# Performance work log

Measured on AMD Instinct MI355X. Metric: run time of the kernel, lower is better.

## Reference

```python
import jax, jax.numpy as jnp
import numpy as np

EMBED_DIM = 768
NUM_HEADS = 12
HEAD_DIM = EMBED_DIM // NUM_HEADS


def setup_inputs() -> dict:
    key = jax.random.key(0)
    ks = jax.random.split(key, 9)
    B, N, D = 8, 1024, EMBED_DIM
    s = 1.0 / np.sqrt(D)
    x = jax.random.normal(ks[0], (B, N, D), dtype=jnp.float32)
    Wq = jax.random.normal(ks[1], (D, D), dtype=jnp.float32) * s
    bq = jnp.zeros((D,), dtype=jnp.float32)
    Wk = jax.random.normal(ks[2], (D, D), dtype=jnp.float32) * s
    bk = jnp.zeros((D,), dtype=jnp.float32)
    Wv = jax.random.normal(ks[3], (D, D), dtype=jnp.float32) * s
    bv = jnp.zeros((D,), dtype=jnp.float32)
    Wo = jax.random.normal(ks[4], (D, D), dtype=jnp.float32) * s
    bo = jnp.zeros((D,), dtype=jnp.float32)
    return {"x": x, "Wq": Wq, "bq": bq, "Wk": Wk, "bk": bk,
            "Wv": Wv, "bv": bv, "Wo": Wo, "bo": bo}


def reference(x, Wq, bq, Wk, bk, Wv, bv, Wo, bo):
    B, N, D = x.shape
    H, Hd = NUM_HEADS, HEAD_DIM
    # torch Linear: y = x @ W.T + b
    q = (x @ Wq.T + bq).reshape(B, N, H, Hd).transpose(0, 2, 1, 3)  # [B,H,N,Hd]
    k = (x @ Wk.T + bk).reshape(B, N, H, Hd).transpose(0, 2, 1, 3)
    v = (x @ Wv.T + bv).reshape(B, N, H, Hd).transpose(0, 2, 1, 3)
    # NOTE: original scales by embed_dim**-0.5 (not head_dim)
    scale = jnp.asarray(D, x.dtype) ** -0.5
    scores = jnp.einsum('bhnd,bhmd->bhnm', q, k) * scale  # [B,H,N,N]
    attn = jax.nn.softmax(scores, axis=-1)
    out = jnp.einsum('bhnm,bhmd->bhnd', attn, v)  # dropout: identity in eval
    out = out.transpose(0, 2, 1, 3).reshape(B, N, D)
    return out @ Wo.T + bo
```

## Files before the change

### kernel.cpp

```cpp
#include <hip/hip_runtime.h>
#include <math.h>


typedef __bf16 bf16x8 __attribute__((ext_vector_type(8)));
typedef float  f32x4  __attribute__((ext_vector_type(4)));
typedef unsigned u32x2 __attribute__((ext_vector_type(2)));
typedef unsigned u32x4 __attribute__((ext_vector_type(4)));
typedef unsigned short ushort_t;

__device__ __forceinline__ unsigned short f2bf(float f) {
    unsigned u = __float_as_uint(f);
    u += 0x7fffu + ((u >> 16) & 1u);
    return (unsigned short)(u >> 16);
}
__device__ __forceinline__ unsigned pk16(unsigned short lo, unsigned short hi) {
    return (unsigned)lo | ((unsigned)hi << 16);
}

#define GLL16(g, l)                                                                        \
    __builtin_amdgcn_global_load_lds((const __attribute__((address_space(1))) void*)(g),   \
                                     (__attribute__((address_space(3))) void*)(l), 16, 0, 0)

__global__ __launch_bounds__(256)
void cast_all(const float* __restrict__ x,
              const float* __restrict__ w0, const float* __restrict__ w1,
              const float* __restrict__ w2, const float* __restrict__ w3,
              ushort_t* __restrict__ xb, ushort_t* __restrict__ wb0,
              ushort_t* __restrict__ wb1, ushort_t* __restrict__ wb2,
              ushort_t* __restrict__ wb3)
{
    const int y = blockIdx.y;
    const float* s; ushort_t* d; int n;
    switch (y) {
        case 0:  s = x;  d = xb;  n = 8192 * 768; break;
        case 1:  s = w0; d = wb0; n = 768 * 768;  break;
        case 2:  s = w1; d = wb1; n = 768 * 768;  break;
        case 3:  s = w2; d = wb2; n = 768 * 768;  break;
        default: s = w3; d = wb3; n = 768 * 768;  break;
    }
    const int i = (blockIdx.x * 256 + threadIdx.x) * 8;
    if (i >= n) return;
    const float4 f0 = *(const float4*)(s + i);
    const float4 f1 = *(const float4*)(s + i + 4);
    ushort4 p0, p1;
    p0.x = f2bf(f0.x); p0.y = f2bf(f0.y); p0.z = f2bf(f0.z); p0.w = f2bf(f0.w);
    p1.x = f2bf(f1.x); p1.y = f2bf(f1.y); p1.z = f2bf(f1.z); p1.w = f2bf(f1.w);
    *(ushort4*)(d + i)     = p0;
    *(ushort4*)(d + i + 4) = p1;
}

__global__ __launch_bounds__(256, 3)
void gemm_qkv(const ushort_t* __restrict__ xb,
              const ushort_t* __restrict__ wqb, const ushort_t* __restrict__ wkb,
              const ushort_t* __restrict__ wvb,
              const float* __restrict__ bq, const float* __restrict__ bk,
              const float* __restrict__ bv,
              ushort_t* __restrict__ Qh, ushort_t* __restrict__ Kl,
              ushort_t* __restrict__ Vl)
{
    __shared__ ushort_t smem[14336];
    ushort_t* As  = smem;
    ushort_t* Ws0 = smem + 2048;
    ushort_t* Ws1 = smem + 6144;
    ushort_t* Ws2 = smem + 10240;

    const int tid = threadIdx.x, L = tid & 63, wv = tid >> 6;
    const int c = L & 15, g = L >> 4;
    const int n0 = blockIdx.x * 128, m0 = blockIdx.y * 64;

    const int qs = ((tid & 3) ^ ((tid >> 3) & 3)) * 8;
    const ushort_t* ap = xb  + (size_t)(m0 + (tid >> 2)) * 768 + qs;
    const ushort_t* wq = wqb + (size_t)(n0 + (tid >> 2)) * 768 + qs;
    const ushort_t* wk = wkb + (size_t)(n0 + (tid >> 2)) * 768 + qs;
    const ushort_t* wvp = wvb + (size_t)(n0 + (tid >> 2)) * 768 + qs;
    const size_t st64 = (size_t)64 * 768;
    const int sg = (g ^ ((c >> 1) & 3)) * 8;

    f32x4 acc[3][4][2];
#pragma unroll
    for (int z = 0; z < 3; ++z)
#pragma unroll
        for (int i = 0; i < 4; ++i)
#pragma unroll
            for (int j = 0; j < 2; ++j) acc[z][i][j] = (f32x4){0.f, 0.f, 0.f, 0.f};

    for (int k0 = 0; k0 < 768; k0 += 32) {
        __syncthreads();
        GLL16(ap + k0,          &As[(size_t)tid * 8]);
        GLL16(wq + k0,          &Ws0[(size_t)tid * 8]);
        GLL16(wq + st64 + k0,   &Ws0[(size_t)(tid + 256) * 8]);
        GLL16(wk + k0,          &Ws1[(size_t)tid * 8]);
        GLL16(wk + st64 + k0,   &Ws1[(size_t)(tid + 256) * 8]);
        GLL16(wvp + k0,         &Ws2[(size_t)tid * 8]);
        GLL16(wvp + st64 + k0,  &Ws2[(size_t)(tid + 256) * 8]);
        __syncthreads();
        bf16x8 af[4];
#pragma unroll
        for (int i = 0; i < 4; ++i)
            af[i] = *(const bf16x8*)&As[(i * 16 + c) * 32 + sg];
        bf16x8 bf[3][2];
        const ushort_t* wsz[3] = {Ws0, Ws1, Ws2};
#pragma unroll
        for (int z = 0; z < 3; ++z)
#pragma unroll
            for (int j = 0; j < 2; ++j)
                bf[z][j] = *(const bf16x8*)&wsz[z][(wv * 32 + j * 16 + c) * 32 + sg];
#pragma unroll
        for (int z = 0; z < 3; ++z)
#pragma unroll
            for (int i = 0; i < 4; ++i)
#pragma unroll
                for (int j = 0; j < 2; ++j)
                    acc[z][i][j] = __builtin_amdgcn_mfma_f32_16x16x32_bf16(
                        af[i], bf[z][j], acc[z][i][j], 0, 0, 0);
    }

    const int b  = m0 >> 10, nb = m0 & 1023;
    const int hcol = n0 + wv * 32;
    const int h = hcol >> 6, uh = (hcol >> 5) & 1;
    const int bh = b * 12 + h;
    ushort_t* scr = smem + wv * 2304;

    float bias2[3][2];
#pragma unroll
    for (int j = 0; j < 2; ++j) {
        bias2[0][j] = bq[hcol + j * 16 + c];
        bias2[1][j] = bk[hcol + j * 16 + c];
        bias2[2][j] = bv[hcol + j * 16 + c];
    }

    __syncthreads();

#pragma unroll
    for (int i = 0; i < 4; ++i)
#pragma unroll
        for (int j = 0; j < 2; ++j)
#pragma unroll
            for (int r = 0; r < 4; ++r)
                scr[(i * 16 + g * 4 + r) * 36 + j * 16 + c] =
                    f2bf(acc[0][i][j][r] + bias2[0][j]);
#pragma unroll
    for (int e = 0; e < 4; ++e) {
        const int slot = e * 64 + L;
        const int row = slot >> 2, ch = slot & 3;
        const u32x4 v = *(const u32x4*)&scr[row * 36 + ch * 8];
        *(u32x4*)&Qh[((size_t)bh * 1024 + nb + row) * 64 + uh * 32 + ch * 8] = v;
    }

#pragma unroll
    for (int i = 0; i < 4; ++i)
#pragma unroll
        for (int j = 0; j < 2; ++j)
#pragma unroll
            for (int r = 0; r < 4; ++r)
                scr[(i * 16 + g * 4 + r) * 36 + j * 16 + c] =
                    f2bf(acc[1][i][j][r] + bias2[1][j]);
#pragma unroll
    for (int tau = 0; tau < 4; ++tau) {
        const u32x4 v = *(const u32x4*)&scr[(tau * 16 + c) * 36 + g * 8];
        *(u32x4*)&Kl[(((size_t)bh * 64 + (nb >> 4) + tau) * 2 + uh) * 512
                     + (size_t)L * 8] = v;
    }

#pragma unroll
    for (int i = 0; i < 4; ++i)
#pragma unroll
        for (int j = 0; j < 2; ++j)
#pragma unroll
            for (int r = 0; r < 4; ++r)
                scr[(j * 16 + c) * 68 + i * 16 + g * 4 + r] =
                    f2bf(acc[2][i][j][r] + bias2[2][j]);
    const int T = nb >> 6;
#pragma unroll
    for (int t = 0; t < 4; ++t) {
        const int htl = t >> 1, u = t & 1;
        const u32x4 v = *(const u32x4*)&scr[(htl * 16 + c) * 68 + u * 32 + g * 8];
        *(u32x4*)&Vl[((((size_t)bh * 4 + uh * 2 + htl) * 16 + T) * 2 + u) * 512
                     + (size_t)L * 8] = v;
    }
}

__global__ __launch_bounds__(256, 3)
void gemm_outp(const ushort_t* __restrict__ attnb, const ushort_t* __restrict__ wob,
               const float* __restrict__ bo, float* __restrict__ out)
{
    __shared__ ushort_t smem[6144];
    ushort_t* As = smem;
    ushort_t* Ws = smem + 2048;
    const int tid = threadIdx.x, L = tid & 63, wv = tid >> 6;
    const int c = L & 15, g = L >> 4;
    const int n0 = blockIdx.x * 128, m0 = blockIdx.y * 64;
    const int qs = ((tid & 3) ^ ((tid >> 3) & 3)) * 8;
    const ushort_t* ap = attnb + (size_t)(m0 + (tid >> 2)) * 768 + qs;
    const ushort_t* wp = wob   + (size_t)(n0 + (tid >> 2)) * 768 + qs;
    const size_t st64 = (size_t)64 * 768;
    const int sg = (g ^ ((c >> 1) & 3)) * 8;

    f32x4 acc[4][2];
#pragma unroll
    for (int i = 0; i < 4; ++i)
#pragma unroll
        for (int j = 0; j < 2; ++j) acc[i][j] = (f32x4){0.f, 0.f, 0.f, 0.f};

    for (int k0 = 0; k0 < 768; k0 += 32) {
        __syncthreads();
        GLL16(ap + k0,        &As[(size_t)tid * 8]);
        GLL16(wp + k0,        &Ws[(size_t)tid * 8]);
        GLL16(wp + st64 + k0, &Ws[(size_t)(tid + 256) * 8]);
        __syncthreads();
        bf16x8 af[4], bf[2];
#pragma unroll
        for (int i = 0; i < 4; ++i)
            af[i] = *(const bf16x8*)&As[(i * 16 + c) * 32 + sg];
#pragma unroll
        for (int j = 0; j < 2; ++j)
            bf[j] = *(const bf16x8*)&Ws[(wv * 32 + j * 16 + c) * 32 + sg];
#pragma unroll
        for (int i = 0; i < 4; ++i)
#pragma unroll
            for (int j = 0; j < 2; ++j)
                acc[i][j] = __builtin_amdgcn_mfma_f32_16x16x32_bf16(
                    af[i], bf[j], acc[i][j], 0, 0, 0);
    }

#pragma unroll
    for (int i = 0; i < 4; ++i) {
        const int row = m0 + i * 16 + g * 4;
#pragma unroll
        for (int j = 0; j < 2; ++j) {
            const int col = n0 + wv * 32 + j * 16 + c;
            const float bsvo = bo[col];
#pragma unroll
            for (int r = 0; r < 4; ++r)
                out[(size_t)(row + r) * 768 + col] = acc[i][j][r] + bsvo;
        }
    }
}

__global__ __launch_bounds__(64, 3)
void flash_bf16(const ushort_t* __restrict__ Q, const ushort_t* __restrict__ Kl,
                const ushort_t* __restrict__ Vl, ushort_t* __restrict__ attnb)
{
    __shared__ ushort_t Ps[2][2][16 * 68];
    const int L = threadIdx.x;
    const int c = L & 15, g = L >> 4;
    const int bh = blockIdx.x, q0 = blockIdx.y * 32;
    const float SC2 = 0.05205954985329743f;

    const ushort_t* Qp = Q + ((size_t)bh * 1024 + q0 + c) * 64 + g * 8;
    bf16x8 qf[2][2];
    qf[0][0] = *(const bf16x8*)Qp;
    qf[0][1] = *(const bf16x8*)(Qp + 32);
    qf[1][0] = *(const bf16x8*)(Qp + 16 * 64);
    qf[1][1] = *(const bf16x8*)(Qp + 16 * 64 + 32);

    const ushort_t* Kb = Kl + (size_t)bh * 65536 + (size_t)L * 8;
    const ushort_t* Vb = Vl + (size_t)bh * 65536 + (size_t)L * 8;

    f32x4 o[2][4];
#pragma unroll
    for (int w = 0; w < 2; ++w)
#pragma unroll
        for (int ht = 0; ht < 4; ++ht) o[w][ht] = (f32x4){0.f, 0.f, 0.f, 0.f};
    float ls[2] = {0.f, 0.f};

    bf16x8 kf0[4], kf1[4];
#pragma unroll
    for (int ct = 0; ct < 4; ++ct) {
        kf0[ct] = *(const bf16x8*)(Kb + (size_t)(ct * 2 + 0) * 512);
        kf1[ct] = *(const bf16x8*)(Kb + (size_t)(ct * 2 + 1) * 512);
    }

    for (int T0 = 0; T0 < 16; T0 += 2) {
#pragma unroll
        for (int p = 0; p < 2; ++p) {
            const int T = T0 + p;
            bf16x8 vf0[4], vf1[4];
#pragma unroll
            for (int ht = 0; ht < 4; ++ht) {
                const ushort_t* vp = Vb + (size_t)((ht * 16 + T) * 2) * 512;
                vf0[ht] = *(const bf16x8*)vp;
                vf1[ht] = *(const bf16x8*)(vp + 512);
            }
            f32x4 s[2][4];
#pragma unroll
            for (int w = 0; w < 2; ++w)
#pragma unroll
                for (int ct = 0; ct < 4; ++ct) {
                    f32x4 zz = (f32x4){0.f, 0.f, 0.f, 0.f};
                    zz = __builtin_amdgcn_mfma_f32_16x16x32_bf16(kf0[ct], qf[w][0], zz, 0, 0, 0);
                    zz = __builtin_amdgcn_mfma_f32_16x16x32_bf16(kf1[ct], qf[w][1], zz, 0, 0, 0);
                    s[w][ct] = zz;
                }
            const int Tn = (T < 15) ? T + 1 : 15;
#pragma unroll
            for (int ct = 0; ct < 4; ++ct) {
                const ushort_t* kp = Kb + (size_t)((Tn * 4 + ct) * 2) * 512;
                kf0[ct] = *(const bf16x8*)kp;
                kf1[ct] = *(const bf16x8*)(kp + 512);
            }
#pragma unroll
            for (int w = 0; w < 2; ++w) {
#pragma unroll
                for (int ct = 0; ct < 4; ++ct) {
                    float pv[4];
#pragma unroll
                    for (int r = 0; r < 4; ++r)
                        pv[r] = __builtin_amdgcn_exp2f(s[w][ct][r] * SC2);
                    ls[w] += (pv[0] + pv[1]) + (pv[2] + pv[3]);
                    const unsigned w01 = __builtin_amdgcn_perm(
                        __float_as_uint(pv[1]), __float_as_uint(pv[0]), 0x07060302u);
                    const unsigned w23 = __builtin_amdgcn_perm(
                        __float_as_uint(pv[3]), __float_as_uint(pv[2]), 0x07060302u);
                    *(u32x2*)&Ps[p][w][c * 68 + ct * 16 + g * 4] = (u32x2){w01, w23};
                }
            }
#pragma unroll
            for (int w = 0; w < 2; ++w) {
                const int pb = c * 68 + g * 8;
                const u32x4 pa  = *(const u32x4*)&Ps[p][w][pb];
                const u32x4 pbv = *(const u32x4*)&Ps[p][w][pb + 32];
                const bf16x8 pf0 = __builtin_bit_cast(bf16x8, pa);
                const bf16x8 pf1 = __builtin_bit_cast(bf16x8, pbv);
#pragma unroll
                for (int ht = 0; ht < 4; ++ht) {
                    o[w][ht] = __builtin_amdgcn_mfma_f32_16x16x32_bf16(vf0[ht], pf0, o[w][ht], 0, 0, 0);
                    o[w][ht] = __builtin_amdgcn_mfma_f32_16x16x32_bf16(vf1[ht], pf1, o[w][ht], 0, 0, 0);
                }
            }
        }
    }

    const int b = bh / 12, h = bh % 12;
#pragma unroll
    for (int w = 0; w < 2; ++w) {
        float l = ls[w];
        l += __shfl_xor(l, 16);
        l += __shfl_xor(l, 32);
        const float inv = 1.f / l;
#pragma unroll
        for (int ht = 0; ht < 4; ++ht) {
            const unsigned w0 = pk16(f2bf(o[w][ht][0] * inv), f2bf(o[w][ht][1] * inv));
            const unsigned w1 = pk16(f2bf(o[w][ht][2] * inv), f2bf(o[w][ht][3] * inv));
            *(u32x2*)&Ps[0][w][c * 68 + ht * 16 + g * 4] = (u32x2){w0, w1};
        }
#pragma unroll
        for (int e = 0; e < 2; ++e) {
            const int row = e * 8 + (L >> 3);
            const int ch  = L & 7;
            const int si  = row * 68 + ch * 8;
            const u32x2 t0 = *(const u32x2*)&Ps[0][w][si];
            const u32x2 t1 = *(const u32x2*)&Ps[0][w][si + 4];
            *(u32x4*)&attnb[((size_t)(b * 1024 + q0 + w * 16 + row)) * 768 + h * 64 + ch * 8]
                = (u32x4){t0.x, t0.y, t1.x, t1.y};
        }
    }
}

extern "C" void kernel_launch(void* const* d_in, const int* in_sizes, int n_in,
                              void* d_out, int out_size, void* d_ws, size_t ws_size,
                              hipStream_t stream)
{
    const float* x  = (const float*)d_in[0];
    const float* Wq = (const float*)d_in[1];
    const float* bq = (const float*)d_in[2];
    const float* Wk = (const float*)d_in[3];
    const float* bk = (const float*)d_in[4];
    const float* Wv = (const float*)d_in[5];
    const float* bv = (const float*)d_in[6];
    const float* Wo = (const float*)d_in[7];
    const float* bo = (const float*)d_in[8];
    float* out = (float*)d_out;

    char* ws = (char*)d_ws;
    ushort_t* xb    = (ushort_t*)(ws);
    ushort_t* wqb   = (ushort_t*)(ws + 12582912);
    ushort_t* wkb   = (ushort_t*)(ws + 12582912 + 1179648);
    ushort_t* wvb   = (ushort_t*)(ws + 12582912 + 2359296);
    ushort_t* wob   = (ushort_t*)(ws + 12582912 + 3538944);
    ushort_t* Qh    = (ushort_t*)(ws + 17301504);
    ushort_t* Kl    = (ushort_t*)(ws + 29884416);
    ushort_t* Vl    = (ushort_t*)(ws + 42467328);
    ushort_t* attnb = (ushort_t*)(ws + 55050240);

    cast_all<<<dim3(3072, 5), 256, 0, stream>>>(x, Wq, Wk, Wv, Wo,
                                                xb, wqb, wkb, wvb, wob);
    gemm_qkv<<<dim3(6, 128), 256, 0, stream>>>(xb, wqb, wkb, wvb,
                                               bq, bk, bv, Qh, Kl, Vl);
    flash_bf16<<<dim3(96, 32), 64, 0, stream>>>(Qh, Kl, Vl, attnb);
    gemm_outp<<<dim3(6, 128), 256, 0, stream>>>(attnb, wob, bo, out);
}
```

Baseline: 197.8 us.

## Pre-tile weights into MFMA fragment layout and load them directly to registers

The weight cast kernel now writes each 768x768 weight in a tiled layout, one 16x32 fragment per 64-lane wave with 8 elements per lane. The QKV and output-projection GEMMs then read their B operands straight from global memory into registers, prefetching the next k-block, instead of staging them through LDS. This shrinks LDS use and removes LDS writes and reads for weights, which may allow higher occupancy. The trade-off is that weight reuse now depends on global and cache bandwidth rather than shared memory.

```diff
diff --git a/kernel.cpp b/kernel.cpp
--- a/kernel.cpp
+++ b/kernel.cpp
@@ -30,23 +30,37 @@
               ushort_t* __restrict__ wb3)
 {
     const int y = blockIdx.y;
-    const float* s; ushort_t* d; int n;
+    if (y == 0) {
+        const int i = (blockIdx.x * 256 + threadIdx.x) * 8;
+        const float4 f0 = *(const float4*)(x + i);
+        const float4 f1 = *(const float4*)(x + i + 4);
+        ushort4 p0, p1;
+        p0.x = f2bf(f0.x); p0.y = f2bf(f0.y); p0.z = f2bf(f0.z); p0.w = f2bf(f0.w);
+        p1.x = f2bf(f1.x); p1.y = f2bf(f1.y); p1.z = f2bf(f1.z); p1.w = f2bf(f1.w);
+        *(ushort4*)(xb + i)     = p0;
+        *(ushort4*)(xb + i + 4) = p1;
+        return;
+    }
+    const int tile = blockIdx.x * 4 + (threadIdx.x >> 6);
+    if (tile >= 48 * 24) return;
+    const float* s; ushort_t* d;
     switch (y) {
-        case 0:  s = x;  d = xb;  n = 8192 * 768; break;
-        case 1:  s = w0; d = wb0; n = 768 * 768;  break;
-        case 2:  s = w1; d = wb1; n = 768 * 768;  break;
-        case 3:  s = w2; d = wb2; n = 768 * 768;  break;
-        default: s = w3; d = wb3; n = 768 * 768;  break;
-    }
-    const int i = (blockIdx.x * 256 + threadIdx.x) * 8;
-    if (i >= n) return;
-    const float4 f0 = *(const float4*)(s + i);
-    const float4 f1 = *(const float4*)(s + i + 4);
+        case 1:  s = w0; d = wb0; break;
+        case 2:  s = w1; d = wb1; break;
+        case 3:  s = w2; d = wb2; break;
+        default: s = w3; d = wb3; break;
+    }
+    const int t = tile / 24, kb = tile % 24;
+    const int L = threadIdx.x & 63, c = L & 15, g = L >> 4;
+    const float* sp = s + (size_t)(t * 16 + c) * 768 + kb * 32 + g * 8;
+    const float4 f0 = *(const float4*)sp;
+    const float4 f1 = *(const float4*)(sp + 4);
     ushort4 p0, p1;
     p0.x = f2bf(f0.x); p0.y = f2bf(f0.y); p0.z = f2bf(f0.z); p0.w = f2bf(f0.w);
     p1.x = f2bf(f1.x); p1.y = f2bf(f1.y); p1.z = f2bf(f1.z); p1.w = f2bf(f1.w);
-    *(ushort4*)(d + i)     = p0;
-    *(ushort4*)(d + i + 4) = p1;
+    ushort_t* dp = d + ((size_t)tile * 64 + L) * 8;
+    *(ushort4*)dp       = p0;
+    *(ushort4*)(dp + 4) = p1;
 }
 
 __global__ __launch_bounds__(256, 3)
@@ -58,24 +72,22 @@
               ushort_t* __restrict__ Qh, ushort_t* __restrict__ Kl,
               ushort_t* __restrict__ Vl)
 {
-    __shared__ ushort_t smem[14336];
-    ushort_t* As  = smem;
-    ushort_t* Ws0 = smem + 2048;
-    ushort_t* Ws1 = smem + 6144;
-    ushort_t* Ws2 = smem + 10240;
+    __shared__ ushort_t smem[9216];
+    ushort_t* As = smem;
 
     const int tid = threadIdx.x, L = tid & 63, wv = tid >> 6;
     const int c = L & 15, g = L >> 4;
     const int n0 = blockIdx.x * 128, m0 = blockIdx.y * 64;
 
     const int qs = ((tid & 3) ^ ((tid >> 3) & 3)) * 8;
-    const ushort_t* ap = xb  + (size_t)(m0 + (tid >> 2)) * 768 + qs;
-    const ushort_t* wq = wqb + (size_t)(n0 + (tid >> 2)) * 768 + qs;
-    const ushort_t* wk = wkb + (size_t)(n0 + (tid >> 2)) * 768 + qs;
-    const ushort_t* wvp = wvb + (size_t)(n0 + (tid >> 2)) * 768 + qs;
-    const size_t st64 = (size_t)64 * 768;
+    const ushort_t* ap = xb + (size_t)(m0 + (tid >> 2)) * 768 + qs;
     const int sg = (g ^ ((c >> 1) & 3)) * 8;
 
+    const size_t wbase = ((size_t)(blockIdx.x * 8 + wv * 2) * 24 * 64 + L) * 8;
+    const ushort_t* wqp = wqb + wbase;
+    const ushort_t* wkp = wkb + wbase;
+    const ushort_t* wvp = wvb + wbase;
+
     f32x4 acc[3][4][2];
 #pragma unroll
     for (int z = 0; z < 3; ++z)
@@ -84,27 +96,22 @@
 #pragma unroll
             for (int j = 0; j < 2; ++j) acc[z][i][j] = (f32x4){0.f, 0.f, 0.f, 0.f};
 
-    for (int k0 = 0; k0 < 768; k0 += 32) {
+    bf16x8 wf[3][2];
+#pragma unroll
+    for (int j = 0; j < 2; ++j) {
+        wf[0][j] = *(const bf16x8*)(wqp + j * 12288);
+        wf[1][j] = *(const bf16x8*)(wkp + j * 12288);
+        wf[2][j] = *(const bf16x8*)(wvp + j * 12288);
+    }
+
+    for (int kb = 0; kb < 24; ++kb) {
         __syncthreads();
-        GLL16(ap + k0,          &As[(size_t)tid * 8]);
-        GLL16(wq + k0,          &Ws0[(size_t)tid * 8]);
-        GLL16(wq + st64 + k0,   &Ws0[(size_t)(tid + 256) * 8]);
-        GLL16(wk + k0,          &Ws1[(size_t)tid * 8]);
-        GLL16(wk + st64 + k0,   &Ws1[(size_t)(tid + 256) * 8]);
-        GLL16(wvp + k0,         &Ws2[(size_t)tid * 8]);
-        GLL16(wvp + st64 + k0,  &Ws2[(size_t)(tid + 256) * 8]);
+        GLL16(ap + kb * 32, &As[(size_t)tid * 8]);
         __syncthreads();
         bf16x8 af[4];
 #pragma unroll
         for (int i = 0; i < 4; ++i)
             af[i] = *(const bf16x8*)&As[(i * 16 + c) * 32 + sg];
-        bf16x8 bf[3][2];
-        const ushort_t* wsz[3] = {Ws0, Ws1, Ws2};
-#pragma unroll
-        for (int z = 0; z < 3; ++z)
-#pragma unroll
-            for (int j = 0; j < 2; ++j)
-                bf[z][j] = *(const bf16x8*)&wsz[z][(wv * 32 + j * 16 + c) * 32 + sg];
 #pragma unroll
         for (int z = 0; z < 3; ++z)
 #pragma unroll
@@ -112,7 +119,14 @@
 #pragma unroll
                 for (int j = 0; j < 2; ++j)
                     acc[z][i][j] = __builtin_amdgcn_mfma_f32_16x16x32_bf16(
-                        af[i], bf[z][j], acc[z][i][j], 0, 0, 0);
+                        af[i], wf[z][j], acc[z][i][j], 0, 0, 0);
+        const int kn = (kb < 23) ? kb + 1 : 23;
+#pragma unroll
+        for (int j = 0; j < 2; ++j) {
+            wf[0][j] = *(const bf16x8*)(wqp + j * 12288 + kn * 512);
+            wf[1][j] = *(const bf16x8*)(wkp + j * 12288 + kn * 512);
+            wf[2][j] = *(const bf16x8*)(wvp + j * 12288 + kn * 512);
+        }
     }
 
     const int b  = m0 >> 10, nb = m0 & 1023;
@@ -184,43 +198,46 @@
 void gemm_outp(const ushort_t* __restrict__ attnb, const ushort_t* __restrict__ wob,
                const float* __restrict__ bo, float* __restrict__ out)
 {
-    __shared__ ushort_t smem[6144];
+    __shared__ ushort_t smem[2048];
     ushort_t* As = smem;
-    ushort_t* Ws = smem + 2048;
     const int tid = threadIdx.x, L = tid & 63, wv = tid >> 6;
     const int c = L & 15, g = L >> 4;
     const int n0 = blockIdx.x * 128, m0 = blockIdx.y * 64;
     const int qs = ((tid & 3) ^ ((tid >> 3) & 3)) * 8;
     const ushort_t* ap = attnb + (size_t)(m0 + (tid >> 2)) * 768 + qs;
-    const ushort_t* wp = wob   + (size_t)(n0 + (tid >> 2)) * 768 + qs;
-    const size_t st64 = (size_t)64 * 768;
     const int sg = (g ^ ((c >> 1) & 3)) * 8;
 
+    const size_t wbase = ((size_t)(blockIdx.x * 8 + wv * 2) * 24 * 64 + L) * 8;
+    const ushort_t* wop = wob + wbase;
+
     f32x4 acc[4][2];
 #pragma unroll
     for (int i = 0; i < 4; ++i)
 #pragma unroll
         for (int j = 0; j < 2; ++j) acc[i][j] = (f32x4){0.f, 0.f, 0.f, 0.f};
 
-    for (int k0 = 0; k0 < 768; k0 += 32) {
+    bf16x8 wf[2];
+#pragma unroll
+    for (int j = 0; j < 2; ++j) wf[j] = *(const bf16x8*)(wop + j * 12288);
+
+    for (int kb = 0; kb < 24; ++kb) {
         __syncthreads();
-        GLL16(ap + k0,        &As[(size_t)tid * 8]);
-        GLL16(wp + k0,        &Ws[(size_t)tid * 8]);
-        GLL16(wp + st64 + k0, &Ws[(size_t)(tid + 256) * 8]);
+        GLL16(ap + kb * 32, &As[(size_t)tid * 8]);
         __syncthreads();
-        bf16x8 af[4], bf[2];
+        bf16x8 af[4];
 #pragma unroll
         for (int i = 0; i < 4; ++i)
             af[i] = *(const bf16x8*)&As[(i * 16 + c) * 32 + sg];
 #pragma unroll
-        for (int j = 0; j < 2; ++j)
-            bf[j] = *(const bf16x8*)&Ws[(wv * 32 + j * 16 + c) * 32 + sg];
-#pragma unroll
         for (int i = 0; i < 4; ++i)
 #pragma unroll
             for (int j = 0; j < 2; ++j)
                 acc[i][j] = __builtin_amdgcn_mfma_f32_16x16x32_bf16(
-                    af[i], bf[j], acc[i][j], 0, 0, 0);
+                    af[i], wf[j], acc[i][j], 0, 0, 0);
+        const int kn = (kb < 23) ? kb + 1 : 23;
+#pragma unroll
+        for (int j = 0; j < 2; ++j)
+            wf[j] = *(const bf16x8*)(wop + j * 12288 + kn * 512);
     }
 
 #pragma unroll
```

After: 188.0 us. 1.05x faster.
